# Performance work log

Measured on AMD Instinct MI355X. Metric: run time of the kernel, lower is better.

## Reference

```python
import jax, jax.numpy as jnp
import numpy as np

EMBED_DIM = 384
NUM_HEADS = 6
HEAD_DIM = EMBED_DIM // NUM_HEADS
SCALE = HEAD_DIM ** -0.5


def setup_inputs() -> dict:
    key = jax.random.key(0)
    k_x, k_qkv_w, k_qkv_b, k_p_w, k_p_b = jax.random.split(key, 5)
    B, N, C = 8, 2048, EMBED_DIM
    x = jax.random.normal(k_x, (B, N, C), dtype=jnp.float32)
    # nn.Linear init ~ U(-1/sqrt(fan_in), 1/sqrt(fan_in)); scaled normal is fine for a reference
    s = 1.0 / np.sqrt(C)
    qkv_w = jax.random.uniform(k_qkv_w, (C, 3 * C), minval=-s, maxval=s, dtype=jnp.float32)
    qkv_b = jax.random.uniform(k_qkv_b, (3 * C,), minval=-s, maxval=s, dtype=jnp.float32)
    proj_w = jax.random.uniform(k_p_w, (C, C), minval=-s, maxval=s, dtype=jnp.float32)
    proj_b = jax.random.uniform(k_p_b, (C,), minval=-s, maxval=s, dtype=jnp.float32)
    return {"x": x, "qkv_w": qkv_w, "qkv_b": qkv_b, "proj_w": proj_w, "proj_b": proj_b}


def reference(x, qkv_w, qkv_b, proj_w, proj_b):
    B, N, C = x.shape
    H, D = NUM_HEADS, C // NUM_HEADS
    qkv = x @ qkv_w + qkv_b                      # [B, N, 3C]
    qkv = qkv.reshape(B, N, 3, H, D)
    q = qkv[:, :, 0].transpose(0, 2, 1, 3)       # [B, H, N, D]
    k = qkv[:, :, 1].transpose(0, 2, 1, 3)
    v = qkv[:, :, 2].transpose(0, 2, 1, 3)
    attn = jnp.einsum('bhnd,bhmd->bhnm', q, k) * SCALE  # [B, H, N, N]
    attn = jax.nn.softmax(attn, axis=-1)
    out = jnp.einsum('bhnm,bhmd->bhnd', attn, v)        # [B, H, N, D]
    out = out.transpose(0, 2, 1, 3).reshape(B, N, C)
    return out @ proj_w + proj_b
```

## Files before the change

### kernel.cpp

```cpp
#include <hip/hip_runtime.h>
#include <hip/hip_bf16.h>
#include <stdint.h>

#define NUM_HEADS 6
#define HEAD_DIM  64
#define EMB       384
#define SEQ       2048
#define NBATCH    8
#define NBH       48
#define QKV_COLS  1152
#define ROWS      16384
#define L2E       1.44269504f

typedef __attribute__((ext_vector_type(8))) short bf16x8;
typedef __attribute__((ext_vector_type(4))) short bf16x4;
typedef __attribute__((ext_vector_type(4))) float f32x4;
typedef __attribute__((ext_vector_type(4))) unsigned int u32x4;

typedef const __attribute__((address_space(1))) void gas_void;
typedef __attribute__((address_space(3))) void las_void;

static __device__ __forceinline__ short f2bf(float f) {
    __hip_bfloat16 h = __float2bfloat16(f);
    return __builtin_bit_cast(short, h);
}
static __device__ __forceinline__ uint32_t pk2(float lo, float hi) {
    return (uint32_t)(uint16_t)f2bf(lo) | ((uint32_t)(uint16_t)f2bf(hi) << 16);
}

__global__ void prep_kernel(const float* __restrict__ x,
                            const float* __restrict__ qkv_w, const float* __restrict__ proj_w,
                            short* __restrict__ Xb, short* __restrict__ qkv_wT, short* __restrict__ proj_wT)
{
    __shared__ float tile[32][33];
    const int id = blockIdx.x, tid = threadIdx.x;
    if (id < 3072) {
        int i = (id * 256 + tid) * 8;
        f32x4 a = *(const f32x4*)&x[i];
        f32x4 b = *(const f32x4*)&x[i + 4];
        bf16x8 o;
        o[0] = f2bf(a[0]); o[1] = f2bf(a[1]); o[2] = f2bf(a[2]); o[3] = f2bf(a[3]);
        o[4] = f2bf(b[0]); o[5] = f2bf(b[1]); o[6] = f2bf(b[2]); o[7] = f2bf(b[3]);
        *(bf16x8*)&Xb[i] = o;
        return;
    }
    const float* in; short* outp; int cols, bx, by;
    if (id < 3504) { in = qkv_w; outp = qkv_wT; cols = QKV_COLS; bx = (id - 3072) % 36; by = (id - 3072) / 36; }
    else           { in = proj_w; outp = proj_wT; cols = EMB;    bx = (id - 3504) % 12; by = (id - 3504) / 12; }
    const int c0 = bx * 32, r0 = by * 32;
    const int xx = tid & 31, yy = tid >> 5;
#pragma unroll
    for (int i = 0; i < 32; i += 8)
        tile[yy + i][xx] = in[(size_t)(r0 + yy + i) * cols + c0 + xx];
    __syncthreads();
#pragma unroll
    for (int i = 0; i < 32; i += 8)
        outp[(size_t)(c0 + yy + i) * EMB + r0 + xx] = f2bf(tile[xx][yy + i]);
}

#define BM 128
#define BN 128
#define BK 64

__global__ __launch_bounds__(256, 2) void qkv_gemm_kernel(
    const short* __restrict__ Xb, const short* __restrict__ WT,
    const float* __restrict__ bias,
    short* __restrict__ Qb, short* __restrict__ Kb, short* __restrict__ Vt)
{
    __shared__ alignas(16) char smem[2][32768];
    const int orig = blockIdx.x;
    const int wgid = (orig & 7) * 144 + (orig >> 3);
    const int m0 = (wgid / 9) * BM;
    const int n0 = (wgid % 9) * BN;
    const int tid = threadIdx.x;
    const int lane = tid & 63, wid = tid >> 6;
    const int wm = wid >> 1, wn = wid & 1;
    const int lr = lane & 15, lg = lane >> 4;
    const char* Xc = (const char*)Xb;
    const char* Wc = (const char*)WT;

    const int t_r = wid * 32 + (lane >> 3);
    const int t_cb = ((lane & 7) * 16) ^ (((lane >> 3) & 7) << 4);

#define GSTAGE(buf, k0)                                                                     \
    do {                                                                                    \
        _Pragma("unroll") for (int i = 0; i < 4; ++i)                                       \
            __builtin_amdgcn_global_load_lds(                                               \
                (gas_void*)(Xc + ((size_t)(m0 + t_r + i * 8)) * (EMB * 2) + (k0) * 2 + t_cb), \
                (las_void*)(&smem[buf][wid * 4096 + i * 1024]), 16, 0, 0);                  \
        _Pragma("unroll") for (int i = 0; i < 4; ++i)                                       \
            __builtin_amdgcn_global_load_lds(                                               \
                (gas_void*)(Wc + ((size_t)(n0 + t_r + i * 8)) * (EMB * 2) + (k0) * 2 + t_cb), \
                (las_void*)(&smem[buf][16384 + wid * 4096 + i * 1024]), 16, 0, 0);          \
    } while (0)

    f32x4 acc[4][4] = {};

    GSTAGE(0, 0);
    __syncthreads();
    for (int t = 0; t < EMB / BK; ++t) {
        const int cur = t & 1;
        if (t + 1 < EMB / BK) GSTAGE(cur ^ 1, (t + 1) * BK);
        const char* Ab = smem[cur];
        const char* Bb = smem[cur] + 16384;
        __builtin_amdgcn_s_setprio(1);
#pragma unroll
        for (int kk = 0; kk < 2; ++kk) {
            bf16x8 af[4], bg[4];
#pragma unroll
            for (int mi = 0; mi < 4; ++mi) {
                const int row = wm * 64 + mi * 16 + lr;
                af[mi] = *(const bf16x8*)(Ab + row * 128 + ((kk * 64 + lg * 16) ^ ((row & 7) << 4)));
            }
#pragma unroll
            for (int ni = 0; ni < 4; ++ni) {
                const int row = wn * 64 + ni * 16 + lr;
                bg[ni] = *(const bf16x8*)(Bb + row * 128 + ((kk * 64 + lg * 16) ^ ((row & 7) << 4)));
            }
#pragma unroll
            for (int mi = 0; mi < 4; ++mi)
#pragma unroll
                for (int ni = 0; ni < 4; ++ni)
                    acc[mi][ni] = __builtin_amdgcn_mfma_f32_16x16x32_bf16(af[mi], bg[ni], acc[mi][ni], 0, 0, 0);
        }
        __builtin_amdgcn_s_setprio(0);
        __syncthreads();
    }
#undef GSTAGE

    const int mat = n0 / EMB;
    if (mat != 2) {
#pragma unroll
        for (int ni = 0; ni < 4; ++ni) {
            int col = n0 + wn * 64 + ni * 16 + lr;
            float bv = bias[col];
            int rem = col - mat * EMB;
            int h = rem >> 6, d = rem & 63;
#pragma unroll
            for (int mi = 0; mi < 4; ++mi) {
#pragma unroll
                for (int j = 0; j < 4; ++j) {
                    int row = m0 + wm * 64 + mi * 16 + lg * 4 + j;
                    int b = row >> 11, n = row & 2047;
                    float v = acc[mi][ni][j] + bv;
                    size_t bh = (size_t)(b * NUM_HEADS + h);
                    if (mat == 0) Qb[(bh * SEQ + n) * HEAD_DIM + d] = f2bf(v * (0.125f * L2E));
                    else          Kb[(bh * SEQ + n) * HEAD_DIM + d] = f2bf(v);
                }
            }
        }
    } else {
        short (*Tt)[136] = (short (*)[136])&smem[0][0];
#pragma unroll
        for (int ni = 0; ni < 4; ++ni) {
            int col = n0 + wn * 64 + ni * 16 + lr;
            float bv = bias[col];
            int c_loc = wn * 64 + ni * 16 + lr;
#pragma unroll
            for (int mi = 0; mi < 4; ++mi) {
                bf16x4 o4;
#pragma unroll
                for (int j = 0; j < 4; ++j)
                    o4[j] = f2bf(acc[mi][ni][j] + bv);
                *(bf16x4*)&Tt[c_loc][wm * 64 + mi * 16 + lg * 4] = o4;
            }
        }
        __syncthreads();
        const int b = m0 >> 11, nbase = m0 & 2047;
        const int d_loc = tid >> 1;
        const int nn = (tid & 1) * 64;
        const int rem = n0 - 2 * EMB + d_loc;
        const int h = rem >> 6, d = rem & 63;
        short* dst = Vt + ((size_t)(b * NUM_HEADS + h) * HEAD_DIM + d) * SEQ + nbase + nn;
#pragma unroll
        for (int e = 0; e < 8; ++e)
            *(bf16x8*)&dst[e * 8] = *(const bf16x8*)&Tt[d_loc][nn + e * 8];
    }
}

__global__ __launch_bounds__(256, 3) void attn_kernel(
    const short* __restrict__ Qb, const short* __restrict__ Kb,
    const short* __restrict__ Vg, short* __restrict__ AO)
{
    __shared__ alignas(16) char Kl[3][8192];
    __shared__ alignas(16) char Vl[3][8192];

    const int orig = blockIdx.x;
    const int wgid = (orig & 7) * 96 + (orig >> 3);
    const int bh = wgid >> 4;
    const int qb = wgid & 15;
    const int tid = threadIdx.x, lane = tid & 63, wid = tid >> 6;
    const int lr = lane & 15, lg = lane >> 4;
    const int q0 = qb * 128 + wid * 32;
    const short* Qh = Qb + (size_t)bh * SEQ * HEAD_DIM;
    const char*  Khc = (const char*)(Kb + (size_t)bh * SEQ * HEAD_DIM);
    const char*  Vhc = (const char*)(Vg + (size_t)bh * HEAD_DIM * SEQ);

    const int s_r0 = wid * 16 + (lane >> 3);
    const int s_cb0 = ((lane & 7) * 16) ^ ((s_r0 & 7) << 4);
    const int s_r1 = s_r0 + 8;
    const int s_cb1 = ((lane & 7) * 16) ^ ((s_r1 & 7) << 4);
    const int p_r0 = ((s_r0 >> 4) & 1) * 32 + ((s_r0 >> 2) & 3) * 8 + ((s_r0 >> 5) & 1) * 4 + (s_r0 & 3);
    const int p_r1 = ((s_r1 >> 4) & 1) * 32 + ((s_r1 >> 2) & 3) * 8 + ((s_r1 >> 5) & 1) * 4 + (s_r1 & 3);

#define STAGE(kp, vp, kbase)                                                            \
    do {                                                                                \
        __builtin_amdgcn_global_load_lds(                                               \
            (gas_void*)(Khc + ((size_t)(kbase) + p_r0) * 128 + s_cb0),                  \
            (las_void*)((kp) + wid * 2048), 16, 0, 0);                                  \
        __builtin_amdgcn_global_load_lds(                                               \
            (gas_void*)(Khc + ((size_t)(kbase) + p_r1) * 128 + s_cb1),                  \
            (las_void*)((kp) + wid * 2048 + 1024), 16, 0, 0);                           \
        __builtin_amdgcn_global_load_lds(                                               \
            (gas_void*)(Vhc + (size_t)s_r0 * (SEQ * 2) + (size_t)(kbase) * 2 + s_cb0),  \
            (las_void*)((vp) + wid * 2048), 16, 0, 0);                                  \
        __builtin_amdgcn_global_load_lds(                                               \
            (gas_void*)(Vhc + (size_t)s_r1 * (SEQ * 2) + (size_t)(kbase) * 2 + s_cb1),  \
            (las_void*)((vp) + wid * 2048 + 1024), 16, 0, 0);                           \
    } while (0)

    bf16x8 qf[2][2];
#pragma unroll
    for (int c2 = 0; c2 < 2; ++c2)
#pragma unroll
        for (int kk = 0; kk < 2; ++kk)
            qf[c2][kk] = *(const bf16x8*)&Qh[(size_t)(q0 + c2 * 16 + lr) * HEAD_DIM + kk * 32 + lg * 8];

    bf16x8 ones;
#pragma unroll
    for (int e = 0; e < 8; ++e) ones[e] = (short)0x3F80;

    f32x4 acc[2][4] = {};
    f32x4 accl[2] = {};

    char *k0p = &Kl[0][0], *k1p = &Kl[1][0], *k2p = &Kl[2][0];
    char *v0p = &Vl[0][0], *v1p = &Vl[1][0], *v2p = &Vl[2][0];

    STAGE(k0p, v0p, 0);
    STAGE(k1p, v1p, 64);
    asm volatile("s_waitcnt vmcnt(4)" ::: "memory");

    for (int t = 0; t < SEQ / 64; ++t) {
        __builtin_amdgcn_s_barrier();
        const int tn = (t + 2 < SEQ / 64 ? t + 2 : SEQ / 64 - 1) * 64;
        STAGE(k2p, v2p, tn);
        asm volatile("s_waitcnt vmcnt(4)" ::: "memory");

        f32x4 s_[2][4] = {};
        __builtin_amdgcn_s_setprio(1);
#pragma unroll
        for (int c = 0; c < 4; ++c) {
            const int row = c * 16 + lr;
            const int sw = (row & 7) << 4;
            bf16x8 kf0 = *(const bf16x8*)(k0p + row * 128 + ((lg * 16) ^ sw));
            bf16x8 kf1 = *(const bf16x8*)(k0p + row * 128 + ((64 + lg * 16) ^ sw));
            s_[0][c] = __builtin_amdgcn_mfma_f32_16x16x32_bf16(kf0, qf[0][0], s_[0][c], 0, 0, 0);
            s_[0][c] = __builtin_amdgcn_mfma_f32_16x16x32_bf16(kf1, qf[0][1], s_[0][c], 0, 0, 0);
            s_[1][c] = __builtin_amdgcn_mfma_f32_16x16x32_bf16(kf0, qf[1][0], s_[1][c], 0, 0, 0);
            s_[1][c] = __builtin_amdgcn_mfma_f32_16x16x32_bf16(kf1, qf[1][1], s_[1][c], 0, 0, 0);
        }
        __builtin_amdgcn_s_setprio(0);

        bf16x8 pb[2][2];
#pragma unroll
        for (int c2 = 0; c2 < 2; ++c2) {
            u32x4 w0, w1;
            w0[0] = pk2(__builtin_amdgcn_exp2f(s_[c2][0][0]), __builtin_amdgcn_exp2f(s_[c2][0][1]));
            w0[1] = pk2(__builtin_amdgcn_exp2f(s_[c2][0][2]), __builtin_amdgcn_exp2f(s_[c2][0][3]));
            w0[2] = pk2(__builtin_amdgcn_exp2f(s_[c2][2][0]), __builtin_amdgcn_exp2f(s_[c2][2][1]));
            w0[3] = pk2(__builtin_amdgcn_exp2f(s_[c2][2][2]), __builtin_amdgcn_exp2f(s_[c2][2][3]));
            w1[0] = pk2(__builtin_amdgcn_exp2f(s_[c2][1][0]), __builtin_amdgcn_exp2f(s_[c2][1][1]));
            w1[1] = pk2(__builtin_amdgcn_exp2f(s_[c2][1][2]), __builtin_amdgcn_exp2f(s_[c2][1][3]));
            w1[2] = pk2(__builtin_amdgcn_exp2f(s_[c2][3][0]), __builtin_amdgcn_exp2f(s_[c2][3][1]));
            w1[3] = pk2(__builtin_amdgcn_exp2f(s_[c2][3][2]), __builtin_amdgcn_exp2f(s_[c2][3][3]));
            pb[c2][0] = __builtin_bit_cast(bf16x8, w0);
            pb[c2][1] = __builtin_bit_cast(bf16x8, w1);
        }

        __builtin_amdgcn_s_setprio(1);
#pragma unroll
        for (int f = 0; f < 4; ++f) {
            const int row = f * 16 + lr;
            const int sw = (row & 7) << 4;
            bf16x8 vf0 = *(const bf16x8*)(v0p + row * 128 + ((lg * 16) ^ sw));
            bf16x8 vf1 = *(const bf16x8*)(v0p + row * 128 + ((64 + lg * 16) ^ sw));
            acc[0][f] = __builtin_amdgcn_mfma_f32_16x16x32_bf16(vf0, pb[0][0], acc[0][f], 0, 0, 0);
            acc[0][f] = __builtin_amdgcn_mfma_f32_16x16x32_bf16(vf1, pb[0][1], acc[0][f], 0, 0, 0);
            acc[1][f] = __builtin_amdgcn_mfma_f32_16x16x32_bf16(vf0, pb[1][0], acc[1][f], 0, 0, 0);
            acc[1][f] = __builtin_amdgcn_mfma_f32_16x16x32_bf16(vf1, pb[1][1], acc[1][f], 0, 0, 0);
        }
        accl[0] = __builtin_amdgcn_mfma_f32_16x16x32_bf16(ones, pb[0][0], accl[0], 0, 0, 0);
        accl[0] = __builtin_amdgcn_mfma_f32_16x16x32_bf16(ones, pb[0][1], accl[0], 0, 0, 0);
        accl[1] = __builtin_amdgcn_mfma_f32_16x16x32_bf16(ones, pb[1][0], accl[1], 0, 0, 0);
        accl[1] = __builtin_amdgcn_mfma_f32_16x16x32_bf16(ones, pb[1][1], accl[1], 0, 0, 0);
        __builtin_amdgcn_s_setprio(0);

        char* kt_ = k0p; k0p = k1p; k1p = k2p; k2p = kt_;
        char* vt_ = v0p; v0p = v1p; v1p = v2p; v2p = vt_;
    }
#undef STAGE

    const int b = bh / NUM_HEADS, h = bh - b * NUM_HEADS;
#pragma unroll
    for (int c2 = 0; c2 < 2; ++c2) {
        const float inv = 1.f / accl[c2][0];
        const size_t rowbase = ((size_t)(b * SEQ + q0 + c2 * 16 + lr)) * EMB + h * HEAD_DIM;
#pragma unroll
        for (int f = 0; f < 4; ++f) {
            bf16x4 o4;
#pragma unroll
            for (int j = 0; j < 4; ++j)
                o4[j] = f2bf(acc[c2][f][j] * inv);
            *(bf16x4*)&AO[rowbase + f * 16 + lg * 4] = o4;
        }
    }
}

__global__ __launch_bounds__(256, 3) void proj_gemm_kernel(
    const short* __restrict__ Ain, const short* __restrict__ WT,
    const float* __restrict__ bias, float* __restrict__ Out)
{
    __shared__ alignas(16) char smem[2][24576];
    const int orig = blockIdx.x;
    const int idx = orig >> 3;
    const int m0 = ((orig & 7) * 32 + idx / 3) * 64;
    const int n0 = (idx % 3) * 128;
    const int tid = threadIdx.x;
    const int lane = tid & 63, wid = tid >> 6;
    const int wm = wid >> 1, wn = wid & 1;
    const int lr = lane & 15, lg = lane >> 4;
    const char* Ac = (const char*)Ain;
    const char* Wc = (const char*)WT;

    const int a_r = wid * 16 + (lane >> 3);
    const int b_r = wid * 32 + (lane >> 3);
    const int t_cb = ((lane & 7) * 16) ^ (((lane >> 3) & 7) << 4);

#define PSTAGE(buf, k0)                                                                     \
    do {                                                                                    \
        _Pragma("unroll") for (int i = 0; i < 2; ++i)                                       \
            __builtin_amdgcn_global_load_lds(                                               \
                (gas_void*)(Ac + ((size_t)(m0 + a_r + i * 8)) * (EMB * 2) + (k0) * 2 + t_cb), \
                (las_void*)(&smem[buf][wid * 2048 + i * 1024]), 16, 0, 0);                  \
        _Pragma("unroll") for (int i = 0; i < 4; ++i)                                       \
            __builtin_amdgcn_global_load_lds(                                               \
                (gas_void*)(Wc + ((size_t)(n0 + b_r + i * 8)) * (EMB * 2) + (k0) * 2 + t_cb), \
                (las_void*)(&smem[buf][8192 + wid * 4096 + i * 1024]), 16, 0, 0);           \
    } while (0)

    f32x4 acc[2][4] = {};

    PSTAGE(0, 0);
    __syncthreads();
    for (int t = 0; t < EMB / BK; ++t) {
        const int cur = t & 1;
        if (t + 1 < EMB / BK) PSTAGE(cur ^ 1, (t + 1) * BK);
        const char* Ab = smem[cur];
        const char* Bb = smem[cur] + 8192;
        __builtin_amdgcn_s_setprio(1);
#pragma unroll
        for (int kk = 0; kk < 2; ++kk) {
            bf16x8 af[2], bg[4];
#pragma unroll
            for (int mi = 0; mi < 2; ++mi) {
                const int row = wm * 32 + mi * 16 + lr;
                af[mi] = *(const bf16x8*)(Ab + row * 128 + ((kk * 64 + lg * 16) ^ ((row & 7) << 4)));
            }
#pragma unroll
            for (int ni = 0; ni < 4; ++ni) {
                const int row = wn * 64 + ni * 16 + lr;
                bg[ni] = *(const bf16x8*)(Bb + row * 128 + ((kk * 64 + lg * 16) ^ ((row & 7) << 4)));
            }
#pragma unroll
            for (int mi = 0; mi < 2; ++mi)
#pragma unroll
                for (int ni = 0; ni < 4; ++ni)
                    acc[mi][ni] = __builtin_amdgcn_mfma_f32_16x16x32_bf16(af[mi], bg[ni], acc[mi][ni], 0, 0, 0);
        }
        __builtin_amdgcn_s_setprio(0);
        __syncthreads();
    }
#undef PSTAGE

#pragma unroll
    for (int ni = 0; ni < 4; ++ni) {
        int col = n0 + wn * 64 + ni * 16 + lr;
        float bv = bias[col];
#pragma unroll
        for (int mi = 0; mi < 2; ++mi)
#pragma unroll
            for (int j = 0; j < 4; ++j) {
                int row = m0 + wm * 32 + mi * 16 + lg * 4 + j;
                Out[(size_t)row * EMB + col] = acc[mi][ni][j] + bv;
            }
    }
}

extern "C" void kernel_launch(void* const* d_in, const int* in_sizes, int n_in,
                              void* d_out, int out_size, void* d_ws, size_t ws_size,
                              hipStream_t stream) {
    const float* x      = (const float*)d_in[0];
    const float* qkv_w  = (const float*)d_in[1];
    const float* qkv_b  = (const float*)d_in[2];
    const float* proj_w = (const float*)d_in[3];
    const float* proj_b = (const float*)d_in[4];
    float* out = (float*)d_out;

    char* ws = (char*)d_ws;
    short* qkv_wT  = (short*)(ws);
    short* proj_wT = (short*)(ws + 884736);
    short* Qb      = (short*)(ws + 1179648);
    short* Kb      = (short*)(ws + 13762560);
    short* Vt      = (short*)(ws + 26345472);
    short* AOXb    = (short*)(ws + 38928384);

    prep_kernel<<<dim3(3648), 256, 0, stream>>>(x, qkv_w, proj_w, AOXb, qkv_wT, proj_wT);
    qkv_gemm_kernel<<<dim3(ROWS / BM * (QKV_COLS / BN)), 256, 0, stream>>>(AOXb, qkv_wT, qkv_b, Qb, Kb, Vt);
    attn_kernel<<<dim3(NBH * (SEQ / 128)), 256, 0, stream>>>(Qb, Kb, Vt, AOXb);
    proj_gemm_kernel<<<dim3(ROWS / 64 * (EMB / 128)), 256, 0, stream>>>(AOXb, proj_wT, proj_b, out);
}
```

Before: 112.1 us.

## Restructure attention into single-wave workgroups with 64 queries per wave

The attention kernel moves from 4-wave workgroups of 32 queries per wave, with a shared triple-buffered K/V tile, to 1-wave workgroups that each handle 64 queries and double-buffer their own K/V tiles. This removes the per-iteration workgroup barrier and doubles MFMA reuse of each K/V fragment loaded from LDS. In exchange each wave issues four times as many global-to-LDS loads per tile, and K/V reuse across waves in a workgroup is lost. Register pressure rises with four query blocks of accumulators, and the prefetch depth drops from two tiles to one.

```diff
diff --git a/kernel.cpp b/kernel.cpp
--- a/kernel.cpp
+++ b/kernel.cpp
@@ -178,50 +178,50 @@
     }
 }
 
-__global__ __launch_bounds__(256, 3) void attn_kernel(
+__global__ __launch_bounds__(64, 1) void attn_kernel(
     const short* __restrict__ Qb, const short* __restrict__ Kb,
     const short* __restrict__ Vg, short* __restrict__ AO)
 {
-    __shared__ alignas(16) char Kl[3][8192];
-    __shared__ alignas(16) char Vl[3][8192];
+    __shared__ alignas(16) char Kl[2][8192];
+    __shared__ alignas(16) char Vl[2][8192];
 
     const int orig = blockIdx.x;
-    const int wgid = (orig & 7) * 96 + (orig >> 3);
-    const int bh = wgid >> 4;
-    const int qb = wgid & 15;
-    const int tid = threadIdx.x, lane = tid & 63, wid = tid >> 6;
+    const int wgid = (orig & 7) * 192 + (orig >> 3);
+    const int bh = wgid >> 5;
+    const int qb = wgid & 31;
+    const int lane = threadIdx.x;
     const int lr = lane & 15, lg = lane >> 4;
-    const int q0 = qb * 128 + wid * 32;
+    const int q0 = qb * 64;
     const short* Qh = Qb + (size_t)bh * SEQ * HEAD_DIM;
     const char*  Khc = (const char*)(Kb + (size_t)bh * SEQ * HEAD_DIM);
     const char*  Vhc = (const char*)(Vg + (size_t)bh * HEAD_DIM * SEQ);
 
-    const int s_r0 = wid * 16 + (lane >> 3);
-    const int s_cb0 = ((lane & 7) * 16) ^ ((s_r0 & 7) << 4);
-    const int s_r1 = s_r0 + 8;
-    const int s_cb1 = ((lane & 7) * 16) ^ ((s_r1 & 7) << 4);
-    const int p_r0 = ((s_r0 >> 4) & 1) * 32 + ((s_r0 >> 2) & 3) * 8 + ((s_r0 >> 5) & 1) * 4 + (s_r0 & 3);
-    const int p_r1 = ((s_r1 >> 4) & 1) * 32 + ((s_r1 >> 2) & 3) * 8 + ((s_r1 >> 5) & 1) * 4 + (s_r1 & 3);
+    const int srow = lane >> 3;
+    const int scb  = ((lane & 7) * 16) ^ (srow << 4);
+    int kpo[8], vpo[8];
+#pragma unroll
+    for (int i = 0; i < 8; ++i) {
+        const int r = i * 8 + srow;
+        const int key = ((r >> 4) & 1) * 32 + ((r >> 2) & 3) * 8 + ((r >> 5) & 1) * 4 + (r & 3);
+        kpo[i] = key * 128 + scb;
+        vpo[i] = r * (SEQ * 2) + scb;
+    }
 
 #define STAGE(kp, vp, kbase)                                                            \
     do {                                                                                \
-        __builtin_amdgcn_global_load_lds(                                               \
-            (gas_void*)(Khc + ((size_t)(kbase) + p_r0) * 128 + s_cb0),                  \
-            (las_void*)((kp) + wid * 2048), 16, 0, 0);                                  \
-        __builtin_amdgcn_global_load_lds(                                               \
-            (gas_void*)(Khc + ((size_t)(kbase) + p_r1) * 128 + s_cb1),                  \
-            (las_void*)((kp) + wid * 2048 + 1024), 16, 0, 0);                           \
-        __builtin_amdgcn_global_load_lds(                                               \
-            (gas_void*)(Vhc + (size_t)s_r0 * (SEQ * 2) + (size_t)(kbase) * 2 + s_cb0),  \
-            (las_void*)((vp) + wid * 2048), 16, 0, 0);                                  \
-        __builtin_amdgcn_global_load_lds(                                               \
-            (gas_void*)(Vhc + (size_t)s_r1 * (SEQ * 2) + (size_t)(kbase) * 2 + s_cb1),  \
-            (las_void*)((vp) + wid * 2048 + 1024), 16, 0, 0);                           \
+        _Pragma("unroll") for (int i = 0; i < 8; ++i)                                   \
+            __builtin_amdgcn_global_load_lds(                                           \
+                (gas_void*)(Khc + (size_t)(kbase) * 128 + kpo[i]),                      \
+                (las_void*)((kp) + i * 1024), 16, 0, 0);                                \
+        _Pragma("unroll") for (int i = 0; i < 8; ++i)                                   \
+            __builtin_amdgcn_global_load_lds(                                           \
+                (gas_void*)(Vhc + (size_t)(kbase) * 2 + vpo[i]),                        \
+                (las_void*)((vp) + i * 1024), 16, 0, 0);                                \
     } while (0)
 
-    bf16x8 qf[2][2];
-#pragma unroll
-    for (int c2 = 0; c2 < 2; ++c2)
+    bf16x8 qf[4][2];
+#pragma unroll
+    for (int c2 = 0; c2 < 4; ++c2)
 #pragma unroll
         for (int kk = 0; kk < 2; ++kk)
             qf[c2][kk] = *(const bf16x8*)&Qh[(size_t)(q0 + c2 * 16 + lr) * HEAD_DIM + kk * 32 + lg * 8];
@@ -230,40 +230,38 @@
 #pragma unroll
     for (int e = 0; e < 8; ++e) ones[e] = (short)0x3F80;
 
-    f32x4 acc[2][4] = {};
-    f32x4 accl[2] = {};
-
-    char *k0p = &Kl[0][0], *k1p = &Kl[1][0], *k2p = &Kl[2][0];
-    char *v0p = &Vl[0][0], *v1p = &Vl[1][0], *v2p = &Vl[2][0];
-
-    STAGE(k0p, v0p, 0);
-    STAGE(k1p, v1p, 64);
-    asm volatile("s_waitcnt vmcnt(4)" ::: "memory");
+    f32x4 acc[4][4] = {};
+    f32x4 accl[4] = {};
+
+    char *cK = &Kl[0][0], *nK = &Kl[1][0];
+    char *cV = &Vl[0][0], *nV = &Vl[1][0];
+
+    STAGE(cK, cV, 0);
 
     for (int t = 0; t < SEQ / 64; ++t) {
-        __builtin_amdgcn_s_barrier();
-        const int tn = (t + 2 < SEQ / 64 ? t + 2 : SEQ / 64 - 1) * 64;
-        STAGE(k2p, v2p, tn);
-        asm volatile("s_waitcnt vmcnt(4)" ::: "memory");
-
-        f32x4 s_[2][4] = {};
+        const int tn = (t + 1 < SEQ / 64 ? t + 1 : SEQ / 64 - 1) * 64;
+        STAGE(nK, nV, tn);
+        asm volatile("s_waitcnt vmcnt(16)" ::: "memory");
+
+        f32x4 s_[4][4] = {};
         __builtin_amdgcn_s_setprio(1);
 #pragma unroll
         for (int c = 0; c < 4; ++c) {
             const int row = c * 16 + lr;
             const int sw = (row & 7) << 4;
-            bf16x8 kf0 = *(const bf16x8*)(k0p + row * 128 + ((lg * 16) ^ sw));
-            bf16x8 kf1 = *(const bf16x8*)(k0p + row * 128 + ((64 + lg * 16) ^ sw));
-            s_[0][c] = __builtin_amdgcn_mfma_f32_16x16x32_bf16(kf0, qf[0][0], s_[0][c], 0, 0, 0);
-            s_[0][c] = __builtin_amdgcn_mfma_f32_16x16x32_bf16(kf1, qf[0][1], s_[0][c], 0, 0, 0);
-            s_[1][c] = __builtin_amdgcn_mfma_f32_16x16x32_bf16(kf0, qf[1][0], s_[1][c], 0, 0, 0);
-            s_[1][c] = __builtin_amdgcn_mfma_f32_16x16x32_bf16(kf1, qf[1][1], s_[1][c], 0, 0, 0);
+            bf16x8 kf0 = *(const bf16x8*)(cK + row * 128 + ((lg * 16) ^ sw));
+            bf16x8 kf1 = *(const bf16x8*)(cK + row * 128 + ((64 + lg * 16) ^ sw));
+#pragma unroll
+            for (int c2 = 0; c2 < 4; ++c2) {
+                s_[c2][c] = __builtin_amdgcn_mfma_f32_16x16x32_bf16(kf0, qf[c2][0], s_[c2][c], 0, 0, 0);
+                s_[c2][c] = __builtin_amdgcn_mfma_f32_16x16x32_bf16(kf1, qf[c2][1], s_[c2][c], 0, 0, 0);
+            }
         }
         __builtin_amdgcn_s_setprio(0);
 
-        bf16x8 pb[2][2];
-#pragma unroll
-        for (int c2 = 0; c2 < 2; ++c2) {
+        bf16x8 pb[4][2];
+#pragma unroll
+        for (int c2 = 0; c2 < 4; ++c2) {
             u32x4 w0, w1;
             w0[0] = pk2(__builtin_amdgcn_exp2f(s_[c2][0][0]), __builtin_amdgcn_exp2f(s_[c2][0][1]));
             w0[1] = pk2(__builtin_amdgcn_exp2f(s_[c2][0][2]), __builtin_amdgcn_exp2f(s_[c2][0][3]));
@@ -282,27 +280,29 @@
         for (int f = 0; f < 4; ++f) {
             const int row = f * 16 + lr;
             const int sw = (row & 7) << 4;
-            bf16x8 vf0 = *(const bf16x8*)(v0p + row * 128 + ((lg * 16) ^ sw));
-            bf16x8 vf1 = *(const bf16x8*)(v0p + row * 128 + ((64 + lg * 16) ^ sw));
-            acc[0][f] = __builtin_amdgcn_mfma_f32_16x16x32_bf16(vf0, pb[0][0], acc[0][f], 0, 0, 0);
-            acc[0][f] = __builtin_amdgcn_mfma_f32_16x16x32_bf16(vf1, pb[0][1], acc[0][f], 0, 0, 0);
-            acc[1][f] = __builtin_amdgcn_mfma_f32_16x16x32_bf16(vf0, pb[1][0], acc[1][f], 0, 0, 0);
-            acc[1][f] = __builtin_amdgcn_mfma_f32_16x16x32_bf16(vf1, pb[1][1], acc[1][f], 0, 0, 0);
-        }
-        accl[0] = __builtin_amdgcn_mfma_f32_16x16x32_bf16(ones, pb[0][0], accl[0], 0, 0, 0);
-        accl[0] = __builtin_amdgcn_mfma_f32_16x16x32_bf16(ones, pb[0][1], accl[0], 0, 0, 0);
-        accl[1] = __builtin_amdgcn_mfma_f32_16x16x32_bf16(ones, pb[1][0], accl[1], 0, 0, 0);
-        accl[1] = __builtin_amdgcn_mfma_f32_16x16x32_bf16(ones, pb[1][1], accl[1], 0, 0, 0);
+            bf16x8 vf0 = *(const bf16x8*)(cV + row * 128 + ((lg * 16) ^ sw));
+            bf16x8 vf1 = *(const bf16x8*)(cV + row * 128 + ((64 + lg * 16) ^ sw));
+#pragma unroll
+            for (int c2 = 0; c2 < 4; ++c2) {
+                acc[c2][f] = __builtin_amdgcn_mfma_f32_16x16x32_bf16(vf0, pb[c2][0], acc[c2][f], 0, 0, 0);
+                acc[c2][f] = __builtin_amdgcn_mfma_f32_16x16x32_bf16(vf1, pb[c2][1], acc[c2][f], 0, 0, 0);
+            }
+        }
+#pragma unroll
+        for (int c2 = 0; c2 < 4; ++c2) {
+            accl[c2] = __builtin_amdgcn_mfma_f32_16x16x32_bf16(ones, pb[c2][0], accl[c2], 0, 0, 0);
+            accl[c2] = __builtin_amdgcn_mfma_f32_16x16x32_bf16(ones, pb[c2][1], accl[c2], 0, 0, 0);
+        }
         __builtin_amdgcn_s_setprio(0);
 
-        char* kt_ = k0p; k0p = k1p; k1p = k2p; k2p = kt_;
-        char* vt_ = v0p; v0p = v1p; v1p = v2p; v2p = vt_;
+        char* tk = cK; cK = nK; nK = tk;
+        char* tv = cV; cV = nV; nV = tv;
     }
 #undef STAGE
 
     const int b = bh / NUM_HEADS, h = bh - b * NUM_HEADS;
 #pragma unroll
-    for (int c2 = 0; c2 < 2; ++c2) {
+    for (int c2 = 0; c2 < 4; ++c2) {
         const float inv = 1.f / accl[c2][0];
         const size_t rowbase = ((size_t)(b * SEQ + q0 + c2 * 16 + lr)) * EMB + h * HEAD_DIM;
 #pragma unroll
@@ -416,6 +416,6 @@
 
     prep_kernel<<<dim3(3648), 256, 0, stream>>>(x, qkv_w, proj_w, AOXb, qkv_wT, proj_wT);
     qkv_gemm_kernel<<<dim3(ROWS / BM * (QKV_COLS / BN)), 256, 0, stream>>>(AOXb, qkv_wT, qkv_b, Qb, Kb, Vt);
-    attn_kernel<<<dim3(NBH * (SEQ / 128)), 256, 0, stream>>>(Qb, Kb, Vt, AOXb);
+    attn_kernel<<<dim3(NBH * (SEQ / 64)), 64, 0, stream>>>(Qb, Kb, Vt, AOXb);
     proj_gemm_kernel<<<dim3(ROWS / 64 * (EMB / 128)), 256, 0, stream>>>(AOXb, proj_wT, proj_b, out);
 }
```

After: 162.4 us. 44.9% more time.
